# Optimization experiments

Measured on AMD Instinct MI355X. Metric: run time of the kernel, lower is better.

The kernel has to match this reference:

```python
import jax, jax.numpy as jnp
import numpy as np

B, S, D, H = 2, 4096, 512, 8
HD = D // H  # head_dim = 64


def setup_inputs() -> dict:
    key = jax.random.key(0)
    ks = jax.random.split(key, 7)
    scale = 1.0 / np.sqrt(D)
    return {
        "x": jax.random.normal(ks[0], (B, S, D), dtype=jnp.float32),
        "Wq": jax.random.uniform(ks[1], (D, D), jnp.float32, -scale, scale),
        "bq": jax.random.uniform(ks[2], (D,), jnp.float32, -scale, scale),
        "Wk": jax.random.uniform(ks[3], (D, D), jnp.float32, -scale, scale),
        "bk": jax.random.uniform(ks[4], (D,), jnp.float32, -scale, scale),
        "Wv": jax.random.uniform(ks[5], (D, D), jnp.float32, -scale, scale),
        "bv": jax.random.uniform(ks[6], (D,), jnp.float32, -scale, scale),
    }


def reference(x, Wq, bq, Wk, bk, Wv, bv):
    # torch Linear: y = x @ W.T + b
    q = x @ Wq.T + bq  # [B,S,D]
    k = x @ Wk.T + bk
    v = x @ Wv.T + bv
    # split heads -> [B,H,S,HD]
    q = q.reshape(B, S, H, HD).transpose(0, 2, 1, 3)
    k = k.reshape(B, S, H, HD).transpose(0, 2, 1, 3)
    v = v.reshape(B, S, H, HD).transpose(0, 2, 1, 3)
    # NOTE: module scales by sqrt(pitch_dim), NOT sqrt(head_dim) -- keep faithful.
    scores = jnp.einsum("bhqd,bhkd->bhqk", q, k) / jnp.sqrt(jnp.float32(D))
    causal = jnp.tril(jnp.ones((S, S), dtype=bool))  # lower-tri incl. diag allowed
    scores = jnp.where(causal, scores, -jnp.inf)
    attn = jax.nn.softmax(scores, axis=-1)
    out = jnp.einsum("bhqk,bhkd->bhqd", attn, v)  # [B,H,S,HD]
    return out.transpose(0, 2, 1, 3).reshape(B, S, D)
```

## Files before the change

kernel.cpp:

```cpp
#include <hip/hip_runtime.h>
#include <hip/hip_bf16.h>
#include <math.h>

#define BB 2
#define SS 4096
#define DD 512
#define HH 8
#define HD 64
#define MSD (BB*SS*DD)
#define WSZ (DD*DD)

#define XOFF (4*(size_t)MSD)
#define WOFF (5*(size_t)MSD)
#define POFF (3*(size_t)MSD)

typedef __attribute__((ext_vector_type(8))) short bf16x8;
typedef __attribute__((ext_vector_type(4))) float f32x4;

__device__ __forceinline__ unsigned short f2bf(float f) {
    unsigned int u = __float_as_uint(f);
    u += 0x7fff + ((u >> 16) & 1);
    return (unsigned short)(u >> 16);
}
__device__ __forceinline__ unsigned int pk2bf(float a, float b) {
    __hip_bfloat162 h = __float22bfloat162_rn(make_float2(a, b));
    union { __hip_bfloat162 h2; unsigned int u; } cv; cv.h2 = h;
    return cv.u;
}

#define GLD16(gsrc, ldst) \
    __builtin_amdgcn_global_load_lds((const __attribute__((address_space(1))) unsigned int*)(gsrc), \
                                     (__attribute__((address_space(3))) unsigned int*)(ldst), 16, 0, 0)

#define CH(qb,t0,t1) ((unsigned)(qb) | ((unsigned)(t0)<<8) | ((unsigned)(t1)<<16))
__device__ __constant__ unsigned int SCHED[48] = {
  CH(31,0,32),  CH(31,32,64), CH(0,0,2),
  CH(15,0,32),  CH(29,0,30),  CH(1,0,4),
  CH(29,30,60), CH(14,0,30),  CH(2,0,6),
  CH(28,0,29),  CH(28,29,58), CH(3,0,8),
  CH(27,0,28),  CH(13,0,28),  CH(4,0,10),
  CH(26,0,27),  CH(26,27,54), CH(5,0,12),
  CH(25,0,26),  CH(12,0,26),  CH(6,0,14),
  CH(24,0,25),  CH(24,25,50), CH(7,0,16),
  CH(30,0,31),  CH(17,0,18),  CH(16,0,17),
  CH(30,31,62), CH(17,18,36), CH(16,17,34),
  CH(27,28,56), CH(19,0,20),  CH(8,0,18),
  CH(25,26,52), CH(20,0,21),  CH(18,0,19),
  CH(23,0,24),  CH(22,0,23),  CH(18,19,38),
  CH(23,24,48), CH(21,0,22),  CH(19,20,40),
  CH(11,0,24),  CH(21,22,44), CH(9,0,20),
  CH(22,23,46), CH(10,0,22),  CH(20,21,42),
};

__global__ __launch_bounds__(256)
void convert_bf16(const float* __restrict__ x,
                  const float* __restrict__ Wq, const float* __restrict__ Wk,
                  const float* __restrict__ Wv, unsigned short* __restrict__ ws) {
    const int i8 = blockIdx.x*256 + threadIdx.x;
    const float* src; unsigned short* dst; size_t off;
    if (i8 < MSD/8) {
        src = x; dst = ws + XOFF; off = (size_t)i8 * 8;
    } else {
        size_t o = ((size_t)i8 - MSD/8) * 8;
        int wsel = (int)(o / WSZ);
        src = (wsel == 0) ? Wq : (wsel == 1) ? Wk : Wv;
        dst = ws + WOFF + (size_t)wsel*WSZ;
        off = o % WSZ;
    }
    float4 a = *(const float4*)&src[off];
    float4 b = *(const float4*)&src[off+4];
    unsigned short r[8] = { f2bf(a.x), f2bf(a.y), f2bf(a.z), f2bf(a.w),
                            f2bf(b.x), f2bf(b.y), f2bf(b.z), f2bf(b.w) };
    *(bf16x8*)&dst[off] = *(const bf16x8*)r;
}

__global__ __launch_bounds__(256)
void qkv_mfma(const float* __restrict__ bq, const float* __restrict__ bk,
              const float* __restrict__ bv, unsigned short* __restrict__ ws) {
    const int z = blockIdx.z;
    const unsigned short* Xb = ws + XOFF;
    const unsigned short* Wb = ws + WOFF + (size_t)z*WSZ;
    const float* bias = (z == 0) ? bq : (z == 1) ? bk : bv;
    unsigned short* dst = ws + (size_t)z*MSD;

    __shared__ __align__(16) unsigned short Sh[2*128*64];
    unsigned short* As = Sh;
    unsigned short* Bs = Sh + 128*64;

    const int tid  = threadIdx.x;
    const int w    = tid >> 6, l = tid & 63;
    const int quad = l >> 4,  r16 = l & 15;
    const int wy   = w >> 1,  wx  = w & 1;
    const int m0   = blockIdx.y * 128;
    const int n0   = blockIdx.x * 128;

    const int srow   = l >> 3;
    const int schunk = (l & 7) ^ srow;

    f32x4 acc[4][4];
    #pragma unroll
    for (int i = 0; i < 4; ++i)
        #pragma unroll
        for (int j = 0; j < 4; ++j) acc[i][j] = (f32x4){0.f,0.f,0.f,0.f};

    for (int k0 = 0; k0 < DD; k0 += 64) {
        __syncthreads();
        #pragma unroll
        for (int u = 0; u < 4; ++u) {
            const int r0 = w*32 + u*8;
            GLD16(&Xb[(size_t)(m0 + r0 + srow)*DD + k0 + schunk*8], &As[r0*64]);
            GLD16(&Wb[(size_t)(n0 + r0 + srow)*DD + k0 + schunk*8], &Bs[r0*64]);
        }
        __syncthreads();
        #pragma unroll
        for (int kc = 0; kc < 2; ++kc) {
            bf16x8 a[4], b[4];
            #pragma unroll
            for (int i = 0; i < 4; ++i) {
                const int mr = wy*64 + i*16 + r16;
                a[i] = *(const bf16x8*)&As[mr*64 + (((kc*4+quad) ^ (mr&7))*8)];
                const int nr = wx*64 + i*16 + r16;
                b[i] = *(const bf16x8*)&Bs[nr*64 + (((kc*4+quad) ^ (nr&7))*8)];
            }
            #pragma unroll
            for (int i = 0; i < 4; ++i)
                #pragma unroll
                for (int j = 0; j < 4; ++j) {
                    if (z == 2)
                        acc[i][j] = __builtin_amdgcn_mfma_f32_16x16x32_bf16(a[i], b[j], acc[i][j], 0, 0, 0);
                    else
                        acc[i][j] = __builtin_amdgcn_mfma_f32_16x16x32_bf16(b[j], a[i], acc[i][j], 0, 0, 0);
                }
        }
    }

    __syncthreads();

    const float qscale = 0.04419417382415922f * 1.4426950408889634f;
    if (z == 2) {
        #pragma unroll
        for (int j = 0; j < 4; ++j) {
            const int nloc = wx*64 + j*16 + r16;
            const float bz = bias[n0 + nloc];
            #pragma unroll
            for (int i = 0; i < 4; ++i) {
                const int chunk = wy*8 + i*2 + (quad>>1);
                const int off   = (quad & 1) * 4;
                unsigned short r4[4];
                #pragma unroll
                for (int reg = 0; reg < 4; ++reg)
                    r4[reg] = f2bf(acc[i][j][reg] + bz);
                *(uint2*)&Sh[nloc*128 + ((chunk ^ (nloc & 7))*8) + off] = *(const uint2*)r4;
            }
        }
    } else {
        #pragma unroll
        for (int j = 0; j < 4; ++j) {
            const int nbase = wx*64 + j*16 + quad*4;
            const float4 bz4 = *(const float4*)&bias[n0 + nbase];
            const int chunk = wx*8 + j*2 + (quad>>1);
            const int off   = (quad & 1) * 4;
            #pragma unroll
            for (int i = 0; i < 4; ++i) {
                const int mloc = wy*64 + i*16 + r16;
                float v0 = acc[i][j][0] + bz4.x;
                float v1 = acc[i][j][1] + bz4.y;
                float v2 = acc[i][j][2] + bz4.z;
                float v3 = acc[i][j][3] + bz4.w;
                if (z == 0) { v0 *= qscale; v1 *= qscale; v2 *= qscale; v3 *= qscale; }
                unsigned short r4[4] = { f2bf(v0), f2bf(v1), f2bf(v2), f2bf(v3) };
                *(uint2*)&Sh[mloc*128 + ((chunk ^ (mloc & 7))*8) + off] = *(const uint2*)r4;
            }
        }
    }
    __syncthreads();

    if (z == 2) {
        const int b_ = m0 >> 12, s0_ = m0 & (SS-1);
        #pragma unroll
        for (int p = 0; p < 8; ++p) {
            const int f = p*256 + tid;
            const int nrow = f >> 4;
            const int mch  = f & 15;
            bf16x8 v = *(const bf16x8*)&Sh[nrow*128 + ((mch ^ (nrow & 7))*8)];
            const int ng = n0 + nrow;
            const int h = ng >> 6, hd = ng & 63;
            *(bf16x8*)&dst[((size_t)(b_*HH + h)*HD + hd)*SS + s0_ + mch*8] = v;
        }
    } else {
        #pragma unroll
        for (int p = 0; p < 8; ++p) {
            const int f = p*256 + tid;
            const int hh  = f >> 10;
            const int rem = f & 1023;
            const int sr  = rem >> 3;
            const int ch  = rem & 7;
            bf16x8 v = *(const bf16x8*)&Sh[sr*128 + (((hh*8 + ch) ^ (sr & 7))*8)];
            const int mg = m0 + sr;
            const int b_ = mg >> 12, s_ = mg & (SS-1);
            const int hg = (n0 >> 6) + hh;
            *(bf16x8*)&dst[((size_t)(b_*HH + hg)*SS + s_)*HD + ch*8] = v;
        }
    }
}

__global__ __launch_bounds__(256)
void attn_mfma(unsigned short* __restrict__ ws, float* __restrict__ out) {
    const int bx = blockIdx.x;
    const int k_ = bx >> 8;
    const int j_ = bx & 255;
    const int bh = j_ & 15;
    const int ti = j_ >> 4;
    const unsigned int e = SCHED[ti*3 + k_];
    const int qb = e & 255;
    const int t0 = (e >> 8) & 255;
    const int t1 = (e >> 16) & 255;
    const int split = !(t0 == 0 && t1 == 2*qb + 2);
    const int half  = (t0 != 0);

    const int tid  = threadIdx.x;
    const int w    = tid >> 6, l = tid & 63;
    const int quad = l >> 4,  r16 = l & 15;
    const int qlo  = qb*128 + w*32;
    const int tdiag = 2*qb + (w >> 1);
    const int qoff  = 32*(w & 1);

    const unsigned short* Qg  = ws;
    const unsigned short* Kg  = ws + (size_t)MSD;
    const unsigned short* Vtg = ws + 2*(size_t)MSD;

    __shared__ __align__(16) unsigned short Ks[2][64*64];
    __shared__ __align__(16) unsigned short Vs[2][64*64];
    __shared__ __align__(16) unsigned int   Ps[4][32*36];
    unsigned int* PsW = Ps[w];

    const size_t kbase = (size_t)bh*SS*HD;
    const size_t vbase = (size_t)bh*HD*SS;

    bf16x8 bqf[2][2];
    #pragma unroll
    for (int nt = 0; nt < 2; ++nt)
        #pragma unroll
        for (int kc = 0; kc < 2; ++kc)
            bqf[nt][kc] = *(const bf16x8*)&Qg[kbase + (size_t)(qlo + nt*16 + r16)*HD + kc*32 + quad*8];

    const f32x4 ZZ = (f32x4){0.f,0.f,0.f,0.f};
    const unsigned short onep[8] = {0x3F80,0x3F80,0x3F80,0x3F80,0x3F80,0x3F80,0x3F80,0x3F80};
    const bf16x8 ones8 = *(const bf16x8*)onep;

    f32x4 od[4][2];
    #pragma unroll
    for (int mt = 0; mt < 4; ++mt)
        #pragma unroll
        for (int nt = 0; nt < 2; ++nt) od[mt][nt] = ZZ;
    f32x4 lacc[2] = {ZZ, ZZ};

    const int sr8 = l >> 3, sc = l & 7;

    {
        const int jb0 = t0*64;
        #pragma unroll
        for (int u = 0; u < 2; ++u) {
            const int row = w*16 + u*8 + sr8;
            const int c   = sc ^ (row & 7);
            GLD16(&Kg [kbase + (size_t)(jb0 + row)*HD + c*8], &Ks[0][(w*16 + u*8)*64]);
            GLD16(&Vtg[vbase + (size_t)row*SS + jb0 + c*8],   &Vs[0][(w*16 + u*8)*64]);
        }
    }

    for (int t = t0; t < t1; ++t) {
        __syncthreads();

        if (t + 1 < t1) {
            const int jb1 = (t + 1)*64;
            const int b1  = (t + 1 - t0) & 1;
            #pragma unroll
            for (int u = 0; u < 2; ++u) {
                const int row = w*16 + u*8 + sr8;
                const int c   = sc ^ (row & 7);
                GLD16(&Kg [kbase + (size_t)(jb1 + row)*HD + c*8], &Ks[b1][(w*16 + u*8)*64]);
                GLD16(&Vtg[vbase + (size_t)row*SS + jb1 + c*8],   &Vs[b1][(w*16 + u*8)*64]);
            }
        }

        if (t <= tdiag) {
            const int bc = (t - t0) & 1;
            const unsigned short* Kb = Ks[bc];
            const unsigned short* Vb = Vs[bc];

            f32x4 z[4][2];
            __builtin_amdgcn_s_setprio(1);
            #pragma unroll
            for (int mt = 0; mt < 4; ++mt) {
                const int row = mt*16 + r16;
                bf16x8 ak0 = *(const bf16x8*)&Kb[row*64 + ((quad     ^ (row&7))*8)];
                bf16x8 ak1 = *(const bf16x8*)&Kb[row*64 + (((4+quad) ^ (row&7))*8)];
                #pragma unroll
                for (int nt = 0; nt < 2; ++nt) {
                    z[mt][nt] = __builtin_amdgcn_mfma_f32_16x16x32_bf16(ak0, bqf[nt][0], ZZ, 0, 0, 0);
                    z[mt][nt] = __builtin_amdgcn_mfma_f32_16x16x32_bf16(ak1, bqf[nt][1], z[mt][nt], 0, 0, 0);
                }
            }
            __builtin_amdgcn_s_setprio(0);

            if (t == tdiag) {
                #pragma unroll
                for (int mt = 0; mt < 4; ++mt)
                    #pragma unroll
                    for (int nt = 0; nt < 2; ++nt)
                        #pragma unroll
                        for (int reg = 0; reg < 4; ++reg)
                            if (mt*16 + quad*4 + reg > qoff + nt*16 + r16)
                                z[mt][nt][reg] = -1e30f;
            }

            #pragma unroll
            for (int mt = 0; mt < 4; ++mt)
                #pragma unroll
                for (int nt = 0; nt < 2; ++nt) {
                    uint2 pk;
                    pk.x = pk2bf(__builtin_amdgcn_exp2f(z[mt][nt][0]),
                                 __builtin_amdgcn_exp2f(z[mt][nt][1]));
                    pk.y = pk2bf(__builtin_amdgcn_exp2f(z[mt][nt][2]),
                                 __builtin_amdgcn_exp2f(z[mt][nt][3]));
                    *(uint2*)&PsW[(nt*16 + r16)*36 + mt*8 + quad*2] = pk;
                }

            asm volatile("s_waitcnt lgkmcnt(0)" ::: "memory");

            bf16x8 pf[2][2];
            #pragma unroll
            for (int nt = 0; nt < 2; ++nt)
                #pragma unroll
                for (int kc = 0; kc < 2; ++kc)
                    pf[nt][kc] = *(const bf16x8*)&PsW[(nt*16 + r16)*36 + kc*16 + quad*4];

            __builtin_amdgcn_s_setprio(1);
            #pragma unroll
            for (int nt = 0; nt < 2; ++nt) {
                lacc[nt] = __builtin_amdgcn_mfma_f32_16x16x32_bf16(ones8, pf[nt][0], lacc[nt], 0, 0, 0);
                lacc[nt] = __builtin_amdgcn_mfma_f32_16x16x32_bf16(ones8, pf[nt][1], lacc[nt], 0, 0, 0);
            }
            #pragma unroll
            for (int mt = 0; mt < 4; ++mt) {
                const int row = mt*16 + r16;
                bf16x8 av0 = *(const bf16x8*)&Vb[row*64 + ((quad     ^ (row&7))*8)];
                bf16x8 av1 = *(const bf16x8*)&Vb[row*64 + (((4+quad) ^ (row&7))*8)];
                #pragma unroll
                for (int nt = 0; nt < 2; ++nt) {
                    od[mt][nt] = __builtin_amdgcn_mfma_f32_16x16x32_bf16(av0, pf[nt][0], od[mt][nt], 0, 0, 0);
                    od[mt][nt] = __builtin_amdgcn_mfma_f32_16x16x32_bf16(av1, pf[nt][1], od[mt][nt], 0, 0, 0);
                }
            }
            __builtin_amdgcn_s_setprio(0);
        }
    }

    if (split) {
        const int p = 2*(bh*16 + (qb - 16)) + half;
        float* Op = (float*)(ws + POFF) + (size_t)p*(128*64);
        float* Lp = (float*)(ws + WOFF) + p*128;
        #pragma unroll
        for (int nt = 0; nt < 2; ++nt) {
            const int qloc = w*32 + nt*16 + r16;
            if (quad == 0) Lp[qloc] = lacc[nt][0];
            #pragma unroll
            for (int mt = 0; mt < 4; ++mt)
                *(f32x4*)&Op[(size_t)qloc*64 + mt*16 + quad*4] = od[mt][nt];
        }
    } else {
        const int b_ = bh >> 3, h = bh & 7;
        #pragma unroll
        for (int nt = 0; nt < 2; ++nt) {
            const float inv = 1.0f / lacc[nt][0];
            const int q = qlo + nt*16 + r16;
            float* op = out + ((size_t)(b_*SS + q))*DD + h*HD;
            #pragma unroll
            for (int mt = 0; mt < 4; ++mt) {
                float4 tt;
                tt.x = od[mt][nt][0]*inv; tt.y = od[mt][nt][1]*inv;
                tt.z = od[mt][nt][2]*inv; tt.w = od[mt][nt][3]*inv;
                *(float4*)&op[mt*16 + quad*4] = tt;
            }
        }
    }
}

__global__ __launch_bounds__(256)
void attn_combine(const unsigned short* __restrict__ ws, float* __restrict__ out) {
    const int i  = blockIdx.x*256 + threadIdx.x;
    const int d4 = i & 15;
    const int q  = (i >> 4) & 127;
    const int r  = i >> 11;
    const int bh = r >> 4, qb = 16 + (r & 15);

    const float* Opart = (const float*)(ws + POFF);
    const float* Lpart = (const float*)(ws + WOFF);

    const float4 a = *(const float4*)&Opart[((size_t)(2*r)*128 + q)*64 + d4*4];
    const float4 b = *(const float4*)&Opart[((size_t)(2*r + 1)*128 + q)*64 + d4*4];
    const float lt = Lpart[(2*r)*128 + q] + Lpart[(2*r + 1)*128 + q];
    const float inv = 1.0f / lt;

    const int qg = qb*128 + q;
    const int b_ = bh >> 3, h = bh & 7;
    float4 o;
    o.x = (a.x + b.x)*inv; o.y = (a.y + b.y)*inv;
    o.z = (a.z + b.z)*inv; o.w = (a.w + b.w)*inv;
    *(float4*)&out[((size_t)(b_*SS + qg))*DD + h*HD + d4*4] = o;
}

extern "C" void kernel_launch(void* const* d_in, const int* in_sizes, int n_in,
                              void* d_out, int out_size, void* d_ws, size_t ws_size,
                              hipStream_t stream) {
    const float* x  = (const float*)d_in[0];
    const float* Wq = (const float*)d_in[1];
    const float* bq = (const float*)d_in[2];
    const float* Wk = (const float*)d_in[3];
    const float* bk = (const float*)d_in[4];
    const float* Wv = (const float*)d_in[5];
    const float* bv = (const float*)d_in[6];
    float* out = (float*)d_out;
    unsigned short* ws = (unsigned short*)d_ws;

    const int nconv = (MSD/8 + 3*WSZ/8 + 255) / 256;
    convert_bf16<<<nconv, 256, 0, stream>>>(x, Wq, Wk, Wv, ws);

    dim3 ggrid(DD/128, (BB*SS)/128, 3);
    qkv_mfma<<<ggrid, 256, 0, stream>>>(bq, bk, bv, ws);

    attn_mfma<<<768, 256, 0, stream>>>(ws, out);
    attn_combine<<<2048, 256, 0, stream>>>(ws, out);
}
```

Baseline: 173.6 us.

## Split long causal rows into finer parts merged via atomics, drop P LDS roundtrip

Replaces the 3-way split schedule with an 80-entry partition table so that query blocks 8 and above are split into roughly equal KV chunks, launching 1280 blocks for finer load balance. Partial outputs and row sums are accumulated with float atomicAdd directly into a pre-zeroed output region and a workspace sum buffer, and a rescale pass then normalizes them. The P matrix transpose through LDS is replaced by v_permlane32/16_swap register shuffles, removing LDS traffic and a wait. Costs include an extra zero-fill kernel, many scalar float atomics, nondeterministic summation order, and a launch-bounds occupancy hint.

```diff
diff --git a/kernel.cpp b/kernel.cpp
--- a/kernel.cpp
+++ b/kernel.cpp
@@ -33,24 +33,59 @@
                                      (__attribute__((address_space(3))) unsigned int*)(ldst), 16, 0, 0)
 
 #define CH(qb,t0,t1) ((unsigned)(qb) | ((unsigned)(t0)<<8) | ((unsigned)(t1)<<16))
-__device__ __constant__ unsigned int SCHED[48] = {
-  CH(31,0,32),  CH(31,32,64), CH(0,0,2),
-  CH(15,0,32),  CH(29,0,30),  CH(1,0,4),
-  CH(29,30,60), CH(14,0,30),  CH(2,0,6),
-  CH(28,0,29),  CH(28,29,58), CH(3,0,8),
-  CH(27,0,28),  CH(13,0,28),  CH(4,0,10),
-  CH(26,0,27),  CH(26,27,54), CH(5,0,12),
-  CH(25,0,26),  CH(12,0,26),  CH(6,0,14),
-  CH(24,0,25),  CH(24,25,50), CH(7,0,16),
-  CH(30,0,31),  CH(17,0,18),  CH(16,0,17),
-  CH(30,31,62), CH(17,18,36), CH(16,17,34),
-  CH(27,28,56), CH(19,0,20),  CH(8,0,18),
-  CH(25,26,52), CH(20,0,21),  CH(18,0,19),
-  CH(23,0,24),  CH(22,0,23),  CH(18,19,38),
-  CH(23,24,48), CH(21,0,22),  CH(19,20,40),
-  CH(11,0,24),  CH(21,22,44), CH(9,0,20),
-  CH(22,23,46), CH(10,0,22),  CH(20,21,42),
+__device__ __constant__ unsigned int PARTS[80] = {
+  CH(31,0,16), CH(31,16,32), CH(31,32,48), CH(31,48,64),
+  CH(30,0,16), CH(30,16,32),
+  CH(23,0,16), CH(23,16,32), CH(23,32,48),
+  CH(22,0,16),
+  CH(15,0,16), CH(15,16,32),
+  CH(7,0,16),
+  CH(30,32,47), CH(30,47,62),
+  CH(29,0,15), CH(29,15,30), CH(29,30,45), CH(29,45,60),
+  CH(28,0,15), CH(28,15,30),
+  CH(22,16,31), CH(22,31,46),
+  CH(21,0,15), CH(21,15,30),
+  CH(14,0,15), CH(14,15,30),
+  CH(28,30,44), CH(28,44,58),
+  CH(27,0,14), CH(27,14,28), CH(27,28,42), CH(27,42,56),
+  CH(26,0,14), CH(26,14,28),
+  CH(21,30,44),
+  CH(20,0,14), CH(20,14,28), CH(20,28,42),
+  CH(19,0,14),
+  CH(13,0,14), CH(13,14,28),
+  CH(6,0,14),
+  CH(26,28,41), CH(26,41,54),
+  CH(25,0,13), CH(25,13,26), CH(25,26,39), CH(25,39,52),
+  CH(24,0,13), CH(24,13,26),
+  CH(19,14,27), CH(19,27,40),
+  CH(18,0,13), CH(18,13,26),
+  CH(12,0,13), CH(12,13,26),
+  CH(24,26,38), CH(24,38,50),
+  CH(18,26,38),
+  CH(17,0,12), CH(17,12,24), CH(17,24,36),
+  CH(16,0,12),
+  CH(11,0,12), CH(11,12,24),
+  CH(5,0,12),
+  CH(16,12,23), CH(16,23,34),
+  CH(10,0,11), CH(10,11,22),
+  CH(9,0,10), CH(9,10,20),
+  CH(4,0,10),
+  CH(8,0,9), CH(8,9,18),
+  CH(3,0,8), CH(2,0,6), CH(1,0,4), CH(0,0,2),
 };
+
+__global__ __launch_bounds__(256)
+void zero_fill(unsigned short* __restrict__ ws, float* __restrict__ out) {
+    const int i = blockIdx.x*256 + threadIdx.x;
+    const float4 z = {0.f, 0.f, 0.f, 0.f};
+    if (i < 393216) {
+        *(float4*)&out[(size_t)524288 + (size_t)i*4] = z;
+    } else if (i < 786432) {
+        *(float4*)&out[(size_t)2621440 + (size_t)(i-393216)*4] = z;
+    } else if (i < 798720) {
+        *(float4*)((float*)(ws + POFF) + (size_t)(i-786432)*4) = z;
+    }
+}
 
 __global__ __launch_bounds__(256)
 void convert_bf16(const float* __restrict__ x,
@@ -204,19 +239,14 @@
     }
 }
 
-__global__ __launch_bounds__(256)
+__global__ __launch_bounds__(256, 5)
 void attn_mfma(unsigned short* __restrict__ ws, float* __restrict__ out) {
     const int bx = blockIdx.x;
-    const int k_ = bx >> 8;
-    const int j_ = bx & 255;
-    const int bh = j_ & 15;
-    const int ti = j_ >> 4;
-    const unsigned int e = SCHED[ti*3 + k_];
+    const int bh = bx & 15;
+    const unsigned int e = PARTS[bx >> 4];
     const int qb = e & 255;
     const int t0 = (e >> 8) & 255;
     const int t1 = (e >> 16) & 255;
-    const int split = !(t0 == 0 && t1 == 2*qb + 2);
-    const int half  = (t0 != 0);
 
     const int tid  = threadIdx.x;
     const int w    = tid >> 6, l = tid & 63;
@@ -231,8 +261,6 @@
 
     __shared__ __align__(16) unsigned short Ks[2][64*64];
     __shared__ __align__(16) unsigned short Vs[2][64*64];
-    __shared__ __align__(16) unsigned int   Ps[4][32*36];
-    unsigned int* PsW = Ps[w];
 
     const size_t kbase = (size_t)bh*SS*HD;
     const size_t vbase = (size_t)bh*HD*SS;
@@ -314,26 +342,31 @@
                                 z[mt][nt][reg] = -1e30f;
             }
 
+            unsigned int X0[4][2], X1[4][2];
             #pragma unroll
             for (int mt = 0; mt < 4; ++mt)
                 #pragma unroll
                 for (int nt = 0; nt < 2; ++nt) {
-                    uint2 pk;
-                    pk.x = pk2bf(__builtin_amdgcn_exp2f(z[mt][nt][0]),
-                                 __builtin_amdgcn_exp2f(z[mt][nt][1]));
-                    pk.y = pk2bf(__builtin_amdgcn_exp2f(z[mt][nt][2]),
-                                 __builtin_amdgcn_exp2f(z[mt][nt][3]));
-                    *(uint2*)&PsW[(nt*16 + r16)*36 + mt*8 + quad*2] = pk;
+                    X0[mt][nt] = pk2bf(__builtin_amdgcn_exp2f(z[mt][nt][0]),
+                                       __builtin_amdgcn_exp2f(z[mt][nt][1]));
+                    X1[mt][nt] = pk2bf(__builtin_amdgcn_exp2f(z[mt][nt][2]),
+                                       __builtin_amdgcn_exp2f(z[mt][nt][3]));
                 }
 
-            asm volatile("s_waitcnt lgkmcnt(0)" ::: "memory");
-
             bf16x8 pf[2][2];
             #pragma unroll
             for (int nt = 0; nt < 2; ++nt)
                 #pragma unroll
-                for (int kc = 0; kc < 2; ++kc)
-                    pf[nt][kc] = *(const bf16x8*)&PsW[(nt*16 + r16)*36 + kc*16 + quad*4];
+                for (int kc = 0; kc < 2; ++kc) {
+                    unsigned int a0 = X0[2*kc][nt], b0 = X0[2*kc+1][nt];
+                    unsigned int a1 = X1[2*kc][nt], b1 = X1[2*kc+1][nt];
+                    asm("v_permlane32_swap_b32 %0, %1" : "+v"(a0), "+v"(b0));
+                    asm("v_permlane16_swap_b32 %0, %1" : "+v"(a0), "+v"(b0));
+                    asm("v_permlane32_swap_b32 %0, %1" : "+v"(a1), "+v"(b1));
+                    asm("v_permlane16_swap_b32 %0, %1" : "+v"(a1), "+v"(b1));
+                    unsigned int wv[4] = { a0, a1, b0, b1 };
+                    pf[nt][kc] = *(const bf16x8*)wv;
+                }
 
             __builtin_amdgcn_s_setprio(1);
             #pragma unroll
@@ -356,20 +389,21 @@
         }
     }
 
-    if (split) {
-        const int p = 2*(bh*16 + (qb - 16)) + half;
-        float* Op = (float*)(ws + POFF) + (size_t)p*(128*64);
-        float* Lp = (float*)(ws + WOFF) + p*128;
+    const int b_ = bh >> 3, h = bh & 7;
+    if (qb >= 8) {
+        float* lbase = (float*)(ws + POFF) + bh*3072 + (qlo - 1024);
         #pragma unroll
         for (int nt = 0; nt < 2; ++nt) {
-            const int qloc = w*32 + nt*16 + r16;
-            if (quad == 0) Lp[qloc] = lacc[nt][0];
+            if (quad == 0) atomicAdd(&lbase[nt*16 + r16], lacc[nt][0]);
+            const int q = qlo + nt*16 + r16;
+            float* op = out + ((size_t)(b_*SS + q))*DD + h*HD;
             #pragma unroll
             for (int mt = 0; mt < 4; ++mt)
-                *(f32x4*)&Op[(size_t)qloc*64 + mt*16 + quad*4] = od[mt][nt];
+                #pragma unroll
+                for (int r = 0; r < 4; ++r)
+                    atomicAdd(&op[mt*16 + quad*4 + r], od[mt][nt][r]);
         }
     } else {
-        const int b_ = bh >> 3, h = bh & 7;
         #pragma unroll
         for (int nt = 0; nt < 2; ++nt) {
             const float inv = 1.0f / lacc[nt][0];
@@ -389,25 +423,16 @@
 __global__ __launch_bounds__(256)
 void attn_combine(const unsigned short* __restrict__ ws, float* __restrict__ out) {
     const int i  = blockIdx.x*256 + threadIdx.x;
-    const int d4 = i & 15;
-    const int q  = (i >> 4) & 127;
-    const int r  = i >> 11;
-    const int bh = r >> 4, qb = 16 + (r & 15);
-
-    const float* Opart = (const float*)(ws + POFF);
-    const float* Lpart = (const float*)(ws + WOFF);
-
-    const float4 a = *(const float4*)&Opart[((size_t)(2*r)*128 + q)*64 + d4*4];
-    const float4 b = *(const float4*)&Opart[((size_t)(2*r + 1)*128 + q)*64 + d4*4];
-    const float lt = Lpart[(2*r)*128 + q] + Lpart[(2*r + 1)*128 + q];
-    const float inv = 1.0f / lt;
-
-    const int qg = qb*128 + q;
+    const int bh = i / 49152;
+    const int rem = i - bh*49152;
+    const int qq = rem >> 4, d4 = rem & 15;
+    const float inv = 1.0f / ((const float*)(ws + POFF))[bh*3072 + qq];
+    const int q  = 1024 + qq;
     const int b_ = bh >> 3, h = bh & 7;
-    float4 o;
-    o.x = (a.x + b.x)*inv; o.y = (a.y + b.y)*inv;
-    o.z = (a.z + b.z)*inv; o.w = (a.w + b.w)*inv;
-    *(float4*)&out[((size_t)(b_*SS + qg))*DD + h*HD + d4*4] = o;
+    float* p = &out[((size_t)(b_*SS + q))*DD + h*HD + d4*4];
+    float4 v = *(const float4*)p;
+    v.x *= inv; v.y *= inv; v.z *= inv; v.w *= inv;
+    *(float4*)p = v;
 }
 
 extern "C" void kernel_launch(void* const* d_in, const int* in_sizes, int n_in,
@@ -423,12 +448,14 @@
     float* out = (float*)d_out;
     unsigned short* ws = (unsigned short*)d_ws;
 
+    zero_fill<<<3120, 256, 0, stream>>>(ws, out);
+
     const int nconv = (MSD/8 + 3*WSZ/8 + 255) / 256;
     convert_bf16<<<nconv, 256, 0, stream>>>(x, Wq, Wk, Wv, ws);
 
     dim3 ggrid(DD/128, (BB*SS)/128, 3);
     qkv_mfma<<<ggrid, 256, 0, stream>>>(bq, bk, bv, ws);
 
-    attn_mfma<<<768, 256, 0, stream>>>(ws, out);
-    attn_combine<<<2048, 256, 0, stream>>>(ws, out);
-}
+    attn_mfma<<<1280, 256, 0, stream>>>(ws, out);
+    attn_combine<<<3072, 256, 0, stream>>>(ws, out);
+}
```

Measured after the change: 388.8 us. 2.24x slower.

## Use 8 waves of 16 queries per attention block and permlane P transpose

Applied to the files above, without the earlier changes.

The attention kernel now runs 512 threads per block, so each wave owns 16 query rows instead of 32. Per-wave register state (accumulators, Q fragments, scores) is halved, and launch bounds ask for higher occupancy. The LDS round-trip used to transpose the P tile into MFMA operand layout is replaced by in-register v_permlane32/16 swaps, which removes the shared P buffer and its wait. The cost is more waves sharing each K/V tile through LDS, and the correctness of the permlane lane mapping has to hold.

```diff
diff --git a/kernel.cpp b/kernel.cpp
--- a/kernel.cpp
+++ b/kernel.cpp
@@ -204,7 +204,7 @@
     }
 }
 
-__global__ __launch_bounds__(256)
+__global__ __launch_bounds__(512, 6)
 void attn_mfma(unsigned short* __restrict__ ws, float* __restrict__ out) {
     const int bx = blockIdx.x;
     const int k_ = bx >> 8;
@@ -221,9 +221,9 @@
     const int tid  = threadIdx.x;
     const int w    = tid >> 6, l = tid & 63;
     const int quad = l >> 4,  r16 = l & 15;
-    const int qlo  = qb*128 + w*32;
-    const int tdiag = 2*qb + (w >> 1);
-    const int qoff  = 32*(w & 1);
+    const int qlo  = qb*128 + w*16;
+    const int tdiag = 2*qb + (w >> 2);
+    const int qoff  = (w & 3)*16;
 
     const unsigned short* Qg  = ws;
     const unsigned short* Kg  = ws + (size_t)MSD;
@@ -231,41 +231,32 @@
 
     __shared__ __align__(16) unsigned short Ks[2][64*64];
     __shared__ __align__(16) unsigned short Vs[2][64*64];
-    __shared__ __align__(16) unsigned int   Ps[4][32*36];
-    unsigned int* PsW = Ps[w];
 
     const size_t kbase = (size_t)bh*SS*HD;
     const size_t vbase = (size_t)bh*HD*SS;
 
-    bf16x8 bqf[2][2];
+    bf16x8 bqf[2];
     #pragma unroll
-    for (int nt = 0; nt < 2; ++nt)
-        #pragma unroll
-        for (int kc = 0; kc < 2; ++kc)
-            bqf[nt][kc] = *(const bf16x8*)&Qg[kbase + (size_t)(qlo + nt*16 + r16)*HD + kc*32 + quad*8];
+    for (int kc = 0; kc < 2; ++kc)
+        bqf[kc] = *(const bf16x8*)&Qg[kbase + (size_t)(qlo + r16)*HD + kc*32 + quad*8];
 
     const f32x4 ZZ = (f32x4){0.f,0.f,0.f,0.f};
     const unsigned short onep[8] = {0x3F80,0x3F80,0x3F80,0x3F80,0x3F80,0x3F80,0x3F80,0x3F80};
     const bf16x8 ones8 = *(const bf16x8*)onep;
 
-    f32x4 od[4][2];
+    f32x4 od[4];
     #pragma unroll
-    for (int mt = 0; mt < 4; ++mt)
-        #pragma unroll
-        for (int nt = 0; nt < 2; ++nt) od[mt][nt] = ZZ;
-    f32x4 lacc[2] = {ZZ, ZZ};
+    for (int mt = 0; mt < 4; ++mt) od[mt] = ZZ;
+    f32x4 lacc = ZZ;
 
     const int sr8 = l >> 3, sc = l & 7;
+    const int srow = w*8 + sr8;
+    const int scol = sc ^ (srow & 7);
 
     {
         const int jb0 = t0*64;
-        #pragma unroll
-        for (int u = 0; u < 2; ++u) {
-            const int row = w*16 + u*8 + sr8;
-            const int c   = sc ^ (row & 7);
-            GLD16(&Kg [kbase + (size_t)(jb0 + row)*HD + c*8], &Ks[0][(w*16 + u*8)*64]);
-            GLD16(&Vtg[vbase + (size_t)row*SS + jb0 + c*8],   &Vs[0][(w*16 + u*8)*64]);
-        }
+        GLD16(&Kg [kbase + (size_t)(jb0 + srow)*HD + scol*8], &Ks[0][(w*8)*64]);
+        GLD16(&Vtg[vbase + (size_t)srow*SS + jb0 + scol*8],   &Vs[0][(w*8)*64]);
     }
 
     for (int t = t0; t < t1; ++t) {
@@ -274,13 +265,8 @@
         if (t + 1 < t1) {
             const int jb1 = (t + 1)*64;
             const int b1  = (t + 1 - t0) & 1;
-            #pragma unroll
-            for (int u = 0; u < 2; ++u) {
-                const int row = w*16 + u*8 + sr8;
-                const int c   = sc ^ (row & 7);
-                GLD16(&Kg [kbase + (size_t)(jb1 + row)*HD + c*8], &Ks[b1][(w*16 + u*8)*64]);
-                GLD16(&Vtg[vbase + (size_t)row*SS + jb1 + c*8],   &Vs[b1][(w*16 + u*8)*64]);
-            }
+            GLD16(&Kg [kbase + (size_t)(jb1 + srow)*HD + scol*8], &Ks[b1][(w*8)*64]);
+            GLD16(&Vtg[vbase + (size_t)srow*SS + jb1 + scol*8],   &Vs[b1][(w*8)*64]);
         }
 
         if (t <= tdiag) {
@@ -288,18 +274,15 @@
             const unsigned short* Kb = Ks[bc];
             const unsigned short* Vb = Vs[bc];
 
-            f32x4 z[4][2];
+            f32x4 z[4];
             __builtin_amdgcn_s_setprio(1);
             #pragma unroll
             for (int mt = 0; mt < 4; ++mt) {
                 const int row = mt*16 + r16;
                 bf16x8 ak0 = *(const bf16x8*)&Kb[row*64 + ((quad     ^ (row&7))*8)];
                 bf16x8 ak1 = *(const bf16x8*)&Kb[row*64 + (((4+quad) ^ (row&7))*8)];
-                #pragma unroll
-                for (int nt = 0; nt < 2; ++nt) {
-                    z[mt][nt] = __builtin_amdgcn_mfma_f32_16x16x32_bf16(ak0, bqf[nt][0], ZZ, 0, 0, 0);
-                    z[mt][nt] = __builtin_amdgcn_mfma_f32_16x16x32_bf16(ak1, bqf[nt][1], z[mt][nt], 0, 0, 0);
-                }
+                z[mt] = __builtin_amdgcn_mfma_f32_16x16x32_bf16(ak0, bqf[0], ZZ, 0, 0, 0);
+                z[mt] = __builtin_amdgcn_mfma_f32_16x16x32_bf16(ak1, bqf[1], z[mt], 0, 0, 0);
             }
             __builtin_amdgcn_s_setprio(0);
 
@@ -307,50 +290,43 @@
                 #pragma unroll
                 for (int mt = 0; mt < 4; ++mt)
                     #pragma unroll
-                    for (int nt = 0; nt < 2; ++nt)
-                        #pragma unroll
-                        for (int reg = 0; reg < 4; ++reg)
-                            if (mt*16 + quad*4 + reg > qoff + nt*16 + r16)
-                                z[mt][nt][reg] = -1e30f;
-            }
-
-            #pragma unroll
-            for (int mt = 0; mt < 4; ++mt)
-                #pragma unroll
-                for (int nt = 0; nt < 2; ++nt) {
-                    uint2 pk;
-                    pk.x = pk2bf(__builtin_amdgcn_exp2f(z[mt][nt][0]),
-                                 __builtin_amdgcn_exp2f(z[mt][nt][1]));
-                    pk.y = pk2bf(__builtin_amdgcn_exp2f(z[mt][nt][2]),
-                                 __builtin_amdgcn_exp2f(z[mt][nt][3]));
-                    *(uint2*)&PsW[(nt*16 + r16)*36 + mt*8 + quad*2] = pk;
-                }
-
-            asm volatile("s_waitcnt lgkmcnt(0)" ::: "memory");
-
-            bf16x8 pf[2][2];
-            #pragma unroll
-            for (int nt = 0; nt < 2; ++nt)
-                #pragma unroll
-                for (int kc = 0; kc < 2; ++kc)
-                    pf[nt][kc] = *(const bf16x8*)&PsW[(nt*16 + r16)*36 + kc*16 + quad*4];
+                    for (int reg = 0; reg < 4; ++reg)
+                        if (mt*16 + quad*4 + reg > qoff + r16)
+                            z[mt][reg] = -1e30f;
+            }
+
+            unsigned int X0[4], X1[4];
+            #pragma unroll
+            for (int mt = 0; mt < 4; ++mt) {
+                X0[mt] = pk2bf(__builtin_amdgcn_exp2f(z[mt][0]),
+                               __builtin_amdgcn_exp2f(z[mt][1]));
+                X1[mt] = pk2bf(__builtin_amdgcn_exp2f(z[mt][2]),
+                               __builtin_amdgcn_exp2f(z[mt][3]));
+            }
+
+            bf16x8 pf[2];
+            #pragma unroll
+            for (int kc = 0; kc < 2; ++kc) {
+                unsigned int a0 = X0[2*kc], b0 = X0[2*kc+1];
+                unsigned int a1 = X1[2*kc], b1 = X1[2*kc+1];
+                asm("v_permlane32_swap_b32 %0, %1" : "+v"(a0), "+v"(b0));
+                asm("v_permlane16_swap_b32 %0, %1" : "+v"(a0), "+v"(b0));
+                asm("v_permlane32_swap_b32 %0, %1" : "+v"(a1), "+v"(b1));
+                asm("v_permlane16_swap_b32 %0, %1" : "+v"(a1), "+v"(b1));
+                unsigned int wv[4] = { a0, a1, b0, b1 };
+                pf[kc] = *(const bf16x8*)wv;
+            }
 
             __builtin_amdgcn_s_setprio(1);
-            #pragma unroll
-            for (int nt = 0; nt < 2; ++nt) {
-                lacc[nt] = __builtin_amdgcn_mfma_f32_16x16x32_bf16(ones8, pf[nt][0], lacc[nt], 0, 0, 0);
-                lacc[nt] = __builtin_amdgcn_mfma_f32_16x16x32_bf16(ones8, pf[nt][1], lacc[nt], 0, 0, 0);
-            }
+            lacc = __builtin_amdgcn_mfma_f32_16x16x32_bf16(ones8, pf[0], lacc, 0, 0, 0);
+            lacc = __builtin_amdgcn_mfma_f32_16x16x32_bf16(ones8, pf[1], lacc, 0, 0, 0);
             #pragma unroll
             for (int mt = 0; mt < 4; ++mt) {
                 const int row = mt*16 + r16;
                 bf16x8 av0 = *(const bf16x8*)&Vb[row*64 + ((quad     ^ (row&7))*8)];
                 bf16x8 av1 = *(const bf16x8*)&Vb[row*64 + (((4+quad) ^ (row&7))*8)];
-                #pragma unroll
-                for (int nt = 0; nt < 2; ++nt) {
-                    od[mt][nt] = __builtin_amdgcn_mfma_f32_16x16x32_bf16(av0, pf[nt][0], od[mt][nt], 0, 0, 0);
-                    od[mt][nt] = __builtin_amdgcn_mfma_f32_16x16x32_bf16(av1, pf[nt][1], od[mt][nt], 0, 0, 0);
-                }
+                od[mt] = __builtin_amdgcn_mfma_f32_16x16x32_bf16(av0, pf[0], od[mt], 0, 0, 0);
+                od[mt] = __builtin_amdgcn_mfma_f32_16x16x32_bf16(av1, pf[1], od[mt], 0, 0, 0);
             }
             __builtin_amdgcn_s_setprio(0);
         }
@@ -360,28 +336,22 @@
         const int p = 2*(bh*16 + (qb - 16)) + half;
         float* Op = (float*)(ws + POFF) + (size_t)p*(128*64);
         float* Lp = (float*)(ws + WOFF) + p*128;
-        #pragma unroll
-        for (int nt = 0; nt < 2; ++nt) {
-            const int qloc = w*32 + nt*16 + r16;
-            if (quad == 0) Lp[qloc] = lacc[nt][0];
-            #pragma unroll
-            for (int mt = 0; mt < 4; ++mt)
-                *(f32x4*)&Op[(size_t)qloc*64 + mt*16 + quad*4] = od[mt][nt];
-        }
+        const int qloc = w*16 + r16;
+        if (quad == 0) Lp[qloc] = lacc[0];
+        #pragma unroll
+        for (int mt = 0; mt < 4; ++mt)
+            *(f32x4*)&Op[(size_t)qloc*64 + mt*16 + quad*4] = od[mt];
     } else {
         const int b_ = bh >> 3, h = bh & 7;
-        #pragma unroll
-        for (int nt = 0; nt < 2; ++nt) {
-            const float inv = 1.0f / lacc[nt][0];
-            const int q = qlo + nt*16 + r16;
-            float* op = out + ((size_t)(b_*SS + q))*DD + h*HD;
-            #pragma unroll
-            for (int mt = 0; mt < 4; ++mt) {
-                float4 tt;
-                tt.x = od[mt][nt][0]*inv; tt.y = od[mt][nt][1]*inv;
-                tt.z = od[mt][nt][2]*inv; tt.w = od[mt][nt][3]*inv;
-                *(float4*)&op[mt*16 + quad*4] = tt;
-            }
+        const float inv = 1.0f / lacc[0];
+        const int q = qlo + r16;
+        float* op = out + ((size_t)(b_*SS + q))*DD + h*HD;
+        #pragma unroll
+        for (int mt = 0; mt < 4; ++mt) {
+            float4 tt;
+            tt.x = od[mt][0]*inv; tt.y = od[mt][1]*inv;
+            tt.z = od[mt][2]*inv; tt.w = od[mt][3]*inv;
+            *(float4*)&op[mt*16 + quad*4] = tt;
         }
     }
 }
@@ -429,6 +399,6 @@
     dim3 ggrid(DD/128, (BB*SS)/128, 3);
     qkv_mfma<<<ggrid, 256, 0, stream>>>(bq, bk, bv, ws);
 
-    attn_mfma<<<768, 256, 0, stream>>>(ws, out);
+    attn_mfma<<<768, 512, 0, stream>>>(ws, out);
     attn_combine<<<2048, 256, 0, stream>>>(ws, out);
 }
```

Result: faster. 166.4 us (-4.2%).

## Split attention key dimension across wave pairs, use permlane for P, register-prefetch W

Applied to the files above, without the earlier changes.

The attention kernel now launches 512 threads per block. Two wave groups each handle half of every 64-key tile and are reduced through shared memory at the end. The P matrix is rebuilt in registers with v_permlane swaps instead of a round trip through LDS. The QKV GEMM now loads weight fragments straight from global memory into registers with one-step prefetch and double-buffers the X tile in LDS, dropping one barrier per k-step. These changes aim for more waves in flight and less LDS traffic, at the cost of a final cross-group reduction and higher register pressure.

```diff
diff --git a/kernel.cpp b/kernel.cpp
--- a/kernel.cpp
+++ b/kernel.cpp
@@ -84,8 +84,6 @@
     unsigned short* dst = ws + (size_t)z*MSD;
 
     __shared__ __align__(16) unsigned short Sh[2*128*64];
-    unsigned short* As = Sh;
-    unsigned short* Bs = Sh + 128*64;
 
     const int tid  = threadIdx.x;
     const int w    = tid >> 6, l = tid & 63;
@@ -103,34 +101,67 @@
         #pragma unroll
         for (int j = 0; j < 4; ++j) acc[i][j] = (f32x4){0.f,0.f,0.f,0.f};
 
-    for (int k0 = 0; k0 < DD; k0 += 64) {
+    const unsigned short* wrow = Wb + (size_t)(n0 + wx*64 + r16)*DD + quad*8;
+
+    #pragma unroll
+    for (int u = 0; u < 4; ++u) {
+        const int r0 = w*32 + u*8;
+        GLD16(&Xb[(size_t)(m0 + r0 + srow)*DD + schunk*8], &Sh[r0*64]);
+    }
+    bf16x8 bfr[2][4];
+    #pragma unroll
+    for (int kc = 0; kc < 2; ++kc)
+        #pragma unroll
+        for (int j = 0; j < 4; ++j)
+            bfr[kc][j] = *(const bf16x8*)(wrow + (size_t)j*(16*DD) + kc*32);
+
+    #pragma unroll
+    for (int kt = 0; kt < 8; ++kt) {
         __syncthreads();
-        #pragma unroll
-        for (int u = 0; u < 4; ++u) {
-            const int r0 = w*32 + u*8;
-            GLD16(&Xb[(size_t)(m0 + r0 + srow)*DD + k0 + schunk*8], &As[r0*64]);
-            GLD16(&Wb[(size_t)(n0 + r0 + srow)*DD + k0 + schunk*8], &Bs[r0*64]);
-        }
-        __syncthreads();
+
+        bf16x8 bnx[2][4];
+        if (kt + 1 < 8) {
+            const int k1 = (kt + 1)*64;
+            const int b1 = (kt + 1) & 1;
+            #pragma unroll
+            for (int u = 0; u < 4; ++u) {
+                const int r0 = w*32 + u*8;
+                GLD16(&Xb[(size_t)(m0 + r0 + srow)*DD + k1 + schunk*8], &Sh[b1*8192 + r0*64]);
+            }
+            #pragma unroll
+            for (int kc = 0; kc < 2; ++kc)
+                #pragma unroll
+                for (int j = 0; j < 4; ++j)
+                    bnx[kc][j] = *(const bf16x8*)(wrow + (size_t)j*(16*DD) + kc*32 + k1);
+        }
+
+        const unsigned short* Asb = Sh + (kt & 1)*8192;
         #pragma unroll
         for (int kc = 0; kc < 2; ++kc) {
-            bf16x8 a[4], b[4];
+            bf16x8 a[4];
             #pragma unroll
             for (int i = 0; i < 4; ++i) {
                 const int mr = wy*64 + i*16 + r16;
-                a[i] = *(const bf16x8*)&As[mr*64 + (((kc*4+quad) ^ (mr&7))*8)];
-                const int nr = wx*64 + i*16 + r16;
-                b[i] = *(const bf16x8*)&Bs[nr*64 + (((kc*4+quad) ^ (nr&7))*8)];
-            }
+                a[i] = *(const bf16x8*)&Asb[mr*64 + (((kc*4+quad) ^ (mr&7))*8)];
+            }
+            __builtin_amdgcn_s_setprio(1);
             #pragma unroll
             for (int i = 0; i < 4; ++i)
                 #pragma unroll
                 for (int j = 0; j < 4; ++j) {
                     if (z == 2)
-                        acc[i][j] = __builtin_amdgcn_mfma_f32_16x16x32_bf16(a[i], b[j], acc[i][j], 0, 0, 0);
+                        acc[i][j] = __builtin_amdgcn_mfma_f32_16x16x32_bf16(a[i], bfr[kc][j], acc[i][j], 0, 0, 0);
                     else
-                        acc[i][j] = __builtin_amdgcn_mfma_f32_16x16x32_bf16(b[j], a[i], acc[i][j], 0, 0, 0);
+                        acc[i][j] = __builtin_amdgcn_mfma_f32_16x16x32_bf16(bfr[kc][j], a[i], acc[i][j], 0, 0, 0);
                 }
+            __builtin_amdgcn_s_setprio(0);
+        }
+        if (kt + 1 < 8) {
+            #pragma unroll
+            for (int kc = 0; kc < 2; ++kc)
+                #pragma unroll
+                for (int j = 0; j < 4; ++j)
+                    bfr[kc][j] = bnx[kc][j];
         }
     }
 
@@ -204,7 +235,7 @@
     }
 }
 
-__global__ __launch_bounds__(256)
+__global__ __launch_bounds__(512, 6)
 void attn_mfma(unsigned short* __restrict__ ws, float* __restrict__ out) {
     const int bx = blockIdx.x;
     const int k_ = bx >> 8;
@@ -221,18 +252,19 @@
     const int tid  = threadIdx.x;
     const int w    = tid >> 6, l = tid & 63;
     const int quad = l >> 4,  r16 = l & 15;
-    const int qlo  = qb*128 + w*32;
-    const int tdiag = 2*qb + (w >> 1);
-    const int qoff  = 32*(w & 1);
+    const int g    = w & 3;
+    const int s    = w >> 2;
+    const int qlo  = qb*128 + g*32;
+    const int tdiag = 2*qb + (g >> 1);
+    const int qoff  = (g & 1)*32;
 
     const unsigned short* Qg  = ws;
     const unsigned short* Kg  = ws + (size_t)MSD;
     const unsigned short* Vtg = ws + 2*(size_t)MSD;
 
-    __shared__ __align__(16) unsigned short Ks[2][64*64];
-    __shared__ __align__(16) unsigned short Vs[2][64*64];
-    __shared__ __align__(16) unsigned int   Ps[4][32*36];
-    unsigned int* PsW = Ps[w];
+    __shared__ __align__(16) unsigned char SMEM[34816];
+    unsigned short* KsB = (unsigned short*)SMEM;
+    unsigned short* VsB = (unsigned short*)(SMEM + 16384);
 
     const size_t kbase = (size_t)bh*SS*HD;
     const size_t vbase = (size_t)bh*HD*SS;
@@ -243,6 +275,11 @@
         #pragma unroll
         for (int kc = 0; kc < 2; ++kc)
             bqf[nt][kc] = *(const bf16x8*)&Qg[kbase + (size_t)(qlo + nt*16 + r16)*HD + kc*32 + quad*8];
+
+    const int x7 = r16 & 7;
+    const unsigned short* pK0 = KsB + s*2048 + r16*64 + ((quad       ^ x7)*8);
+    const unsigned short* pK1 = KsB + s*2048 + r16*64 + (((4+quad)   ^ x7)*8);
+    const unsigned short* pV  = VsB +          r16*64 + (((s*4+quad) ^ x7)*8);
 
     const f32x4 ZZ = (f32x4){0.f,0.f,0.f,0.f};
     const unsigned short onep[8] = {0x3F80,0x3F80,0x3F80,0x3F80,0x3F80,0x3F80,0x3F80,0x3F80};
@@ -250,22 +287,19 @@
 
     f32x4 od[4][2];
     #pragma unroll
-    for (int mt = 0; mt < 4; ++mt)
-        #pragma unroll
-        for (int nt = 0; nt < 2; ++nt) od[mt][nt] = ZZ;
+    for (int mtd = 0; mtd < 4; ++mtd)
+        #pragma unroll
+        for (int nt = 0; nt < 2; ++nt) od[mtd][nt] = ZZ;
     f32x4 lacc[2] = {ZZ, ZZ};
 
     const int sr8 = l >> 3, sc = l & 7;
+    const int srow = w*8 + sr8;
+    const int scol = sc ^ (srow & 7);
 
     {
         const int jb0 = t0*64;
-        #pragma unroll
-        for (int u = 0; u < 2; ++u) {
-            const int row = w*16 + u*8 + sr8;
-            const int c   = sc ^ (row & 7);
-            GLD16(&Kg [kbase + (size_t)(jb0 + row)*HD + c*8], &Ks[0][(w*16 + u*8)*64]);
-            GLD16(&Vtg[vbase + (size_t)row*SS + jb0 + c*8],   &Vs[0][(w*16 + u*8)*64]);
-        }
+        GLD16(&Kg [kbase + (size_t)(jb0 + srow)*HD + scol*8], &KsB[(w*8)*64]);
+        GLD16(&Vtg[vbase + (size_t)srow*SS + jb0 + scol*8],   &VsB[(w*8)*64]);
     }
 
     for (int t = t0; t < t1; ++t) {
@@ -274,113 +308,123 @@
         if (t + 1 < t1) {
             const int jb1 = (t + 1)*64;
             const int b1  = (t + 1 - t0) & 1;
-            #pragma unroll
-            for (int u = 0; u < 2; ++u) {
-                const int row = w*16 + u*8 + sr8;
-                const int c   = sc ^ (row & 7);
-                GLD16(&Kg [kbase + (size_t)(jb1 + row)*HD + c*8], &Ks[b1][(w*16 + u*8)*64]);
-                GLD16(&Vtg[vbase + (size_t)row*SS + jb1 + c*8],   &Vs[b1][(w*16 + u*8)*64]);
-            }
+            GLD16(&Kg [kbase + (size_t)(jb1 + srow)*HD + scol*8], &KsB[b1*4096 + (w*8)*64]);
+            GLD16(&Vtg[vbase + (size_t)srow*SS + jb1 + scol*8],   &VsB[b1*4096 + (w*8)*64]);
         }
 
         if (t <= tdiag) {
-            const int bc = (t - t0) & 1;
-            const unsigned short* Kb = Ks[bc];
-            const unsigned short* Vb = Vs[bc];
-
-            f32x4 z[4][2];
+            const int boff = ((t - t0) & 1) * 4096;
+
+            f32x4 z[2][2];
             __builtin_amdgcn_s_setprio(1);
             #pragma unroll
-            for (int mt = 0; mt < 4; ++mt) {
-                const int row = mt*16 + r16;
-                bf16x8 ak0 = *(const bf16x8*)&Kb[row*64 + ((quad     ^ (row&7))*8)];
-                bf16x8 ak1 = *(const bf16x8*)&Kb[row*64 + (((4+quad) ^ (row&7))*8)];
+            for (int mm = 0; mm < 2; ++mm) {
+                bf16x8 ak0 = *(const bf16x8*)(pK0 + boff + mm*1024);
+                bf16x8 ak1 = *(const bf16x8*)(pK1 + boff + mm*1024);
                 #pragma unroll
                 for (int nt = 0; nt < 2; ++nt) {
-                    z[mt][nt] = __builtin_amdgcn_mfma_f32_16x16x32_bf16(ak0, bqf[nt][0], ZZ, 0, 0, 0);
-                    z[mt][nt] = __builtin_amdgcn_mfma_f32_16x16x32_bf16(ak1, bqf[nt][1], z[mt][nt], 0, 0, 0);
+                    z[mm][nt] = __builtin_amdgcn_mfma_f32_16x16x32_bf16(ak0, bqf[nt][0], ZZ, 0, 0, 0);
+                    z[mm][nt] = __builtin_amdgcn_mfma_f32_16x16x32_bf16(ak1, bqf[nt][1], z[mm][nt], 0, 0, 0);
                 }
             }
             __builtin_amdgcn_s_setprio(0);
 
             if (t == tdiag) {
                 #pragma unroll
-                for (int mt = 0; mt < 4; ++mt)
+                for (int mm = 0; mm < 2; ++mm)
                     #pragma unroll
                     for (int nt = 0; nt < 2; ++nt)
                         #pragma unroll
                         for (int reg = 0; reg < 4; ++reg)
-                            if (mt*16 + quad*4 + reg > qoff + nt*16 + r16)
-                                z[mt][nt][reg] = -1e30f;
-            }
-
-            #pragma unroll
-            for (int mt = 0; mt < 4; ++mt)
+                            if ((2*s + mm)*16 + quad*4 + reg > qoff + nt*16 + r16)
+                                z[mm][nt][reg] = -1e30f;
+            }
+
+            unsigned int X0[2][2], X1[2][2];
+            #pragma unroll
+            for (int mm = 0; mm < 2; ++mm)
                 #pragma unroll
                 for (int nt = 0; nt < 2; ++nt) {
-                    uint2 pk;
-                    pk.x = pk2bf(__builtin_amdgcn_exp2f(z[mt][nt][0]),
-                                 __builtin_amdgcn_exp2f(z[mt][nt][1]));
-                    pk.y = pk2bf(__builtin_amdgcn_exp2f(z[mt][nt][2]),
-                                 __builtin_amdgcn_exp2f(z[mt][nt][3]));
-                    *(uint2*)&PsW[(nt*16 + r16)*36 + mt*8 + quad*2] = pk;
+                    X0[mm][nt] = pk2bf(__builtin_amdgcn_exp2f(z[mm][nt][0]),
+                                       __builtin_amdgcn_exp2f(z[mm][nt][1]));
+                    X1[mm][nt] = pk2bf(__builtin_amdgcn_exp2f(z[mm][nt][2]),
+                                       __builtin_amdgcn_exp2f(z[mm][nt][3]));
                 }
 
-            asm volatile("s_waitcnt lgkmcnt(0)" ::: "memory");
-
-            bf16x8 pf[2][2];
+            bf16x8 pf[2];
+            #pragma unroll
+            for (int nt = 0; nt < 2; ++nt) {
+                unsigned int a0 = X0[0][nt], b0 = X0[1][nt];
+                unsigned int a1 = X1[0][nt], b1 = X1[1][nt];
+                asm("v_permlane32_swap_b32 %0, %1" : "+v"(a0), "+v"(b0));
+                asm("v_permlane16_swap_b32 %0, %1" : "+v"(a0), "+v"(b0));
+                asm("v_permlane32_swap_b32 %0, %1" : "+v"(a1), "+v"(b1));
+                asm("v_permlane16_swap_b32 %0, %1" : "+v"(a1), "+v"(b1));
+                unsigned int wv[4] = { a0, a1, b0, b1 };
+                pf[nt] = *(const bf16x8*)wv;
+            }
+
+            __builtin_amdgcn_s_setprio(1);
+            lacc[0] = __builtin_amdgcn_mfma_f32_16x16x32_bf16(ones8, pf[0], lacc[0], 0, 0, 0);
+            lacc[1] = __builtin_amdgcn_mfma_f32_16x16x32_bf16(ones8, pf[1], lacc[1], 0, 0, 0);
+            #pragma unroll
+            for (int mtd = 0; mtd < 4; ++mtd) {
+                bf16x8 av = *(const bf16x8*)(pV + boff + mtd*1024);
+                od[mtd][0] = __builtin_amdgcn_mfma_f32_16x16x32_bf16(av, pf[0], od[mtd][0], 0, 0, 0);
+                od[mtd][1] = __builtin_amdgcn_mfma_f32_16x16x32_bf16(av, pf[1], od[mtd][1], 0, 0, 0);
+            }
+            __builtin_amdgcn_s_setprio(0);
+        }
+    }
+
+    __syncthreads();
+    if (s == 1) {
+        #pragma unroll
+        for (int mtd = 0; mtd < 4; ++mtd)
             #pragma unroll
             for (int nt = 0; nt < 2; ++nt)
-                #pragma unroll
-                for (int kc = 0; kc < 2; ++kc)
-                    pf[nt][kc] = *(const bf16x8*)&PsW[(nt*16 + r16)*36 + kc*16 + quad*4];
-
-            __builtin_amdgcn_s_setprio(1);
+                *(f32x4*)(SMEM + (size_t)(mtd*2+nt)*4096 + (g*64 + l)*16) = od[mtd][nt];
+        float2 lx; lx.x = lacc[0][0]; lx.y = lacc[1][0];
+        *(float2*)(SMEM + 32768 + (g*64 + l)*8) = lx;
+    }
+    __syncthreads();
+    if (s == 0) {
+        #pragma unroll
+        for (int mtd = 0; mtd < 4; ++mtd)
             #pragma unroll
             for (int nt = 0; nt < 2; ++nt) {
-                lacc[nt] = __builtin_amdgcn_mfma_f32_16x16x32_bf16(ones8, pf[nt][0], lacc[nt], 0, 0, 0);
-                lacc[nt] = __builtin_amdgcn_mfma_f32_16x16x32_bf16(ones8, pf[nt][1], lacc[nt], 0, 0, 0);
-            }
-            #pragma unroll
-            for (int mt = 0; mt < 4; ++mt) {
-                const int row = mt*16 + r16;
-                bf16x8 av0 = *(const bf16x8*)&Vb[row*64 + ((quad     ^ (row&7))*8)];
-                bf16x8 av1 = *(const bf16x8*)&Vb[row*64 + (((4+quad) ^ (row&7))*8)];
-                #pragma unroll
-                for (int nt = 0; nt < 2; ++nt) {
-                    od[mt][nt] = __builtin_amdgcn_mfma_f32_16x16x32_bf16(av0, pf[nt][0], od[mt][nt], 0, 0, 0);
-                    od[mt][nt] = __builtin_amdgcn_mfma_f32_16x16x32_bf16(av1, pf[nt][1], od[mt][nt], 0, 0, 0);
+                f32x4 o2 = *(const f32x4*)(SMEM + (size_t)(mtd*2+nt)*4096 + (g*64 + l)*16);
+                od[mtd][nt] += o2;
+            }
+        float2 lx = *(const float2*)(SMEM + 32768 + (g*64 + l)*8);
+        lacc[0][0] += lx.x; lacc[1][0] += lx.y;
+
+        if (split) {
+            const int p = 2*(bh*16 + (qb - 16)) + half;
+            float* Op = (float*)(ws + POFF) + (size_t)p*(128*64);
+            float* Lp = (float*)(ws + WOFF) + p*128;
+            #pragma unroll
+            for (int nt = 0; nt < 2; ++nt) {
+                const int qloc = g*32 + nt*16 + r16;
+                if (quad == 0) Lp[qloc] = lacc[nt][0];
+                #pragma unroll
+                for (int mtd = 0; mtd < 4; ++mtd)
+                    *(f32x4*)&Op[(size_t)qloc*64 + mtd*16 + quad*4] = od[mtd][nt];
+            }
+        } else {
+            const int b_ = bh >> 3, h = bh & 7;
+            #pragma unroll
+            for (int nt = 0; nt < 2; ++nt) {
+                const float inv = 1.0f / lacc[nt][0];
+                const int q = qlo + nt*16 + r16;
+                float* op = out + ((size_t)(b_*SS + q))*DD + h*HD;
+                #pragma unroll
+                for (int mtd = 0; mtd < 4; ++mtd) {
+                    float4 tt;
+                    tt.x = od[mtd][nt][0]*inv; tt.y = od[mtd][nt][1]*inv;
+                    tt.z = od[mtd][nt][2]*inv; tt.w = od[mtd][nt][3]*inv;
+                    *(float4*)&op[mtd*16 + quad*4] = tt;
                 }
-            }
-            __builtin_amdgcn_s_setprio(0);
-        }
-    }
-
-    if (split) {
-        const int p = 2*(bh*16 + (qb - 16)) + half;
-        float* Op = (float*)(ws + POFF) + (size_t)p*(128*64);
-        float* Lp = (float*)(ws + WOFF) + p*128;
-        #pragma unroll
-        for (int nt = 0; nt < 2; ++nt) {
-            const int qloc = w*32 + nt*16 + r16;
-            if (quad == 0) Lp[qloc] = lacc[nt][0];
-            #pragma unroll
-            for (int mt = 0; mt < 4; ++mt)
-                *(f32x4*)&Op[(size_t)qloc*64 + mt*16 + quad*4] = od[mt][nt];
-        }
-    } else {
-        const int b_ = bh >> 3, h = bh & 7;
-        #pragma unroll
-        for (int nt = 0; nt < 2; ++nt) {
-            const float inv = 1.0f / lacc[nt][0];
-            const int q = qlo + nt*16 + r16;
-            float* op = out + ((size_t)(b_*SS + q))*DD + h*HD;
-            #pragma unroll
-            for (int mt = 0; mt < 4; ++mt) {
-                float4 tt;
-                tt.x = od[mt][nt][0]*inv; tt.y = od[mt][nt][1]*inv;
-                tt.z = od[mt][nt][2]*inv; tt.w = od[mt][nt][3]*inv;
-                *(float4*)&op[mt*16 + quad*4] = tt;
             }
         }
     }
@@ -429,6 +473,6 @@
     dim3 ggrid(DD/128, (BB*SS)/128, 3);
     qkv_mfma<<<ggrid, 256, 0, stream>>>(bq, bk, bv, ws);
 
-    attn_mfma<<<768, 256, 0, stream>>>(ws, out);
+    attn_mfma<<<768, 512, 0, stream>>>(ws, out);
     attn_combine<<<2048, 256, 0, stream>>>(ws, out);
 }
```

New measurement: 320.9 us. 1.85x slower.
